# Performance work log

Measured on AMD Instinct MI355X. Metric: run time of the kernel, lower is better.

The kernel has to match this reference:

```python
import jax, jax.numpy as jnp
import numpy as np

N = 256    # b_s == nq == h*q == h*v (forced by the module's reshape/matmul constraints)
A = 1024   # model dim 'a'
K_DIM = 1  # self.k (h*k must equal 1 for the .view to be valid)


def setup_inputs() -> dict:
    key = jax.random.key(0)
    ks = jax.random.split(key, 5)
    s = 0.02
    x = jax.random.normal(ks[0], (N, N, A), dtype=jnp.float32)
    Wq = jax.random.normal(ks[1], (N, A), dtype=jnp.float32) * s      # fc_q: a -> h*q = N
    bq = jnp.zeros((N,), dtype=jnp.float32)
    Wk = jax.random.normal(ks[2], (K_DIM, A), dtype=jnp.float32) * s  # fc_k: a -> h*k = 1
    bk = jnp.zeros((K_DIM,), dtype=jnp.float32)
    Wv = jax.random.normal(ks[3], (N, A), dtype=jnp.float32) * s      # fc_v: a -> h*v = N
    bv = jnp.zeros((N,), dtype=jnp.float32)
    Wo = jax.random.normal(ks[4], (A, N), dtype=jnp.float32) * s      # fc_o: h*v -> a
    bo = jnp.zeros((A,), dtype=jnp.float32)
    return {"x": x, "Wq": Wq, "bq": bq, "Wk": Wk, "bk": bk,
            "Wv": Wv, "bv": bv, "Wo": Wo, "bo": bo}


def reference(x, Wq, bq, Wk, bk, Wv, bv, Wo, bo):
    # q = fc_q(x): (b_s, nq, h*q)
    q = jnp.einsum('bna,qa->bnq', x, Wq) + bq
    # k = fc_k(x).view(b_s, nq).permute(1, 0): (nq, b_s)
    klin = (jnp.einsum('bna,ka->bnk', x, Wk) + bk)[..., 0]  # (b_s, nq)
    kT = klin.T                                             # (nq, b_s)
    # att = matmul(kT, q) / sqrt(self.k): 2D kT broadcast over batch of q
    att = jnp.einsum('nm,bmq->bnq', kT, q) / np.sqrt(np.float32(K_DIM))
    att = jax.nn.softmax(att, axis=-1)  # dropout = identity (eval mode)
    # v = fc_v(x): (b_s, nq, h*v)
    v = jnp.einsum('bna,va->bnv', x, Wv) + bv
    # out = matmul(v, att): batched (nq, h*v) @ (nq, h*q) with h*v == nq
    out = jnp.einsum('bnm,bmq->bnq', v, att)
    # fc_o: (..., h*v) -> (..., a)
    return jnp.einsum('bnv,av->bna', out, Wo) + bo
```

## Files before the change

kernel.cpp:

```cpp
#include <hip/hip_runtime.h>


typedef unsigned short u16;
typedef unsigned int   uint;
using f32x4  = __attribute__((ext_vector_type(4))) float;
using bf16x8 = __attribute__((ext_vector_type(8))) short;
using u16x4  = __attribute__((ext_vector_type(4))) u16;

#define DEVI static __device__ __forceinline__

DEVI u16 f2bf(float f){
  union { float f; uint u; } v; v.f = f;
  uint r = v.u + 0x7fffu + ((v.u >> 16) & 1u);
  return (u16)(r >> 16);
}
DEVI float bf2f(u16 h){
  union { uint u; float f; } v; v.u = ((uint)h) << 16;
  return v.f;
}

typedef const uint __attribute__((address_space(1)))* as1_cuintp;
typedef uint __attribute__((address_space(3)))* as3_uintp;

DEVI void gl_lds16(const void* g, void* l){
  __builtin_amdgcn_global_load_lds((as1_cuintp)g, (as3_uintp)l, 16, 0, 0);
}

template<int ROWS, int NW>
DEVI void stage_tile(const u16* __restrict__ g, long long rowStride,
                     u16* lds, int lane, int wave){
  constexpr int NLD = ROWS >> 3;
  #pragma unroll
  for (int j = 0; j < NLD/NW; ++j){
    int r0  = (wave + NW*j) << 3;
    int row = r0 + (lane >> 3);
    const u16* src = g + (long long)row * rowStride
                       + (((lane & 7) ^ (lane >> 3)) << 3);
    gl_lds16(src, lds + r0 * 64);
  }
}

DEVI bf16x8 ldfrag(const u16* s, int rbase, int kk, int lane){
  int row = rbase + (lane & 15);
  int c   = (kk << 2) + (lane >> 4);
  return *(const bf16x8*)(s + row*64 + ((c ^ (row & 7)) << 3));
}

__global__ __launch_bounds__(512, 2)
void k_qvkl(const float* __restrict__ x,
            const u16* __restrict__ Wqh, const u16* __restrict__ Wql,
            const u16* __restrict__ Wvh,
            const float* __restrict__ Wk, const float* __restrict__ bk,
            const float* __restrict__ bq, const float* __restrict__ bv,
            u16* __restrict__ qTh, u16* __restrict__ qTl,
            u16* __restrict__ vout,
            u16* __restrict__ klTh, u16* __restrict__ klTl)
{
  __shared__ __align__(16) u16 sX [128*64];
  __shared__ __align__(16) u16 sXl[128*64];
  __shared__ __align__(16) u16 sQh[256*64];
  __shared__ __align__(16) u16 sQl[256*64];
  __shared__ __align__(16) u16 sV [256*64];

  const int tid  = threadIdx.x;
  const int lane = tid & 63;
  const int wave = tid >> 6;
  const int wm   = wave >> 2;
  const int wn   = wave & 3;
  const int tileM = blockIdx.x << 7;

  f32x4 qacc[4][4], vacc[4][4];
  #pragma unroll
  for (int i=0;i<4;i++)
    #pragma unroll
    for (int j=0;j<4;j++){
      qacc[i][j][0]=0.f; qacc[i][j][1]=0.f; qacc[i][j][2]=0.f; qacc[i][j][3]=0.f;
      vacc[i][j][0]=0.f; vacc[i][j][1]=0.f; vacc[i][j][2]=0.f; vacc[i][j][3]=0.f;
    }
  float kacc[4] = {0.f, 0.f, 0.f, 0.f};

  f32x4 xr[4];
  #pragma unroll
  for (int j=0;j<4;j++){
    int f = tid + (j << 9);
    xr[j] = *(const f32x4*)(x + (long long)(tileM + (f >> 4))*1024 + ((f & 15) << 2));
  }

  for (int kt = 0; kt < 1024; kt += 64){
    #pragma unroll
    for (int j=0;j<4;j++){
      int f   = tid + (j << 9);
      int row = f >> 4;
      int c16 = f & 15;
      f32x4 t = xr[j];
      u16x4 h4, l4;
      #pragma unroll
      for (int e=0;e<4;e++){
        u16 h = f2bf(t[e]);
        h4[e] = h;
        l4[e] = f2bf(t[e] - bf2f(h));
      }
      int off = row*64 + (((c16 >> 1) ^ (row & 7)) << 3) + ((c16 & 1) << 2);
      *(u16x4*)(sX  + off) = h4;
      *(u16x4*)(sXl + off) = l4;
      f32x4 w = *(const f32x4*)(Wk + kt + (c16 << 2));
      kacc[j] += t[0]*w[0] + t[1]*w[1] + t[2]*w[2] + t[3]*w[3];
    }
    stage_tile<256,8>(Wqh + kt, 1024, sQh, lane, wave);
    stage_tile<256,8>(Wql + kt, 1024, sQl, lane, wave);
    stage_tile<256,8>(Wvh + kt, 1024, sV , lane, wave);
    __syncthreads();

    if (kt < 960){
      #pragma unroll
      for (int j=0;j<4;j++){
        int f = tid + (j << 9);
        xr[j] = *(const f32x4*)(x + (long long)(tileM + (f >> 4))*1024
                                + (kt + 64) + ((f & 15) << 2));
      }
    }

    #pragma unroll
    for (int kk=0;kk<2;kk++){
      bf16x8 a[4], al[4];
      #pragma unroll
      for (int i=0;i<4;i++){
        a[i]  = ldfrag(sX , wm*64 + i*16, kk, lane);
        al[i] = ldfrag(sXl, wm*64 + i*16, kk, lane);
      }
      {
        bf16x8 b[4];
        #pragma unroll
        for (int i=0;i<4;i++) b[i] = ldfrag(sQh, wn*64 + i*16, kk, lane);
        #pragma unroll
        for (int mt=0;mt<4;mt++)
          #pragma unroll
          for (int nt=0;nt<4;nt++){
            qacc[mt][nt] = __builtin_amdgcn_mfma_f32_16x16x32_bf16(a[mt],  b[nt], qacc[mt][nt], 0,0,0);
            qacc[mt][nt] = __builtin_amdgcn_mfma_f32_16x16x32_bf16(al[mt], b[nt], qacc[mt][nt], 0,0,0);
          }
      }
      {
        bf16x8 b[4];
        #pragma unroll
        for (int i=0;i<4;i++) b[i] = ldfrag(sQl, wn*64 + i*16, kk, lane);
        #pragma unroll
        for (int mt=0;mt<4;mt++)
          #pragma unroll
          for (int nt=0;nt<4;nt++)
            qacc[mt][nt] = __builtin_amdgcn_mfma_f32_16x16x32_bf16(a[mt], b[nt], qacc[mt][nt], 0,0,0);
      }
      {
        bf16x8 b[4];
        #pragma unroll
        for (int i=0;i<4;i++) b[i] = ldfrag(sV, wn*64 + i*16, kk, lane);
        #pragma unroll
        for (int mt=0;mt<4;mt++)
          #pragma unroll
          for (int nt=0;nt<4;nt++)
            vacc[mt][nt] = __builtin_amdgcn_mfma_f32_16x16x32_bf16(a[mt], b[nt], vacc[mt][nt], 0,0,0);
      }
    }
    __syncthreads();
  }

  #pragma unroll
  for (int j=0;j<4;j++){
    #pragma unroll
    for (int m=1;m<16;m<<=1) kacc[j] += __shfl_xor(kacc[j], m, 64);
  }
  if ((lane & 15) == 0){
    #pragma unroll
    for (int j=0;j<4;j++){
      int f = tid + (j << 9);
      int r = tileM + (f >> 4);
      float kv = kacc[j] + bk[0];
      u16 h = f2bf(kv);
      klTh[(r & 255)*256 + (r >> 8)] = h;
      klTl[(r & 255)*256 + (r >> 8)] = f2bf(kv - bf2f(h));
    }
  }

  #pragma unroll
  for (int mt=0;mt<4;mt++)
    #pragma unroll
    for (int nt=0;nt<4;nt++){
      const int gr = tileM + wm*64 + mt*16 + ((lane >> 4) << 2);
      const int gc = wn*64 + nt*16 + (lane & 15);
      {
        const int bidx = gr >> 8, m = gr & 255;
        const long long off = ((long long)bidx << 16) + ((long long)gc << 8) + m;
        const float bb = bq[gc];
        u16x4 h4, l4;
        f32x4 v = qacc[mt][nt];
        #pragma unroll
        for (int r=0;r<4;r++){
          float fq = v[r] + bb;
          u16 h = f2bf(fq);
          h4[r] = h;
          l4[r] = f2bf(fq - bf2f(h));
        }
        *(u16x4*)(qTh + off) = h4;
        *(u16x4*)(qTl + off) = l4;
      }
      {
        const float bb = bv[gc];
        u16* o = vout + (long long)gr * 256 + gc;
        f32x4 v = vacc[mt][nt];
        #pragma unroll
        for (int r=0;r<4;r++) o[(long long)r * 256] = f2bf(v[r] + bb);
      }
    }
}

template<int WMODE>
__global__ __launch_bounds__(256, 2)
void k_gemm(const u16* __restrict__ Ag,
            const u16* __restrict__ Bhg,
            int N, int K, int tnCount, long long bStrideB,
            const float* __restrict__ bias,
            void* __restrict__ Co)
{
  __shared__ __align__(16) u16 sA[128*64];
  __shared__ __align__(16) u16 sB[128*64];

  const int tid  = threadIdx.x;
  const int lane = tid & 63;
  const int wave = tid >> 6;
  const int wm   = wave >> 1;
  const int wn   = wave & 1;
  const int tn   = blockIdx.x % tnCount;
  const int tm   = blockIdx.x / tnCount;
  const int tileM = tm << 7;
  const int tileN = tn << 7;

  const long long bOff = bStrideB ? (long long)(tileM >> 8) * bStrideB : 0;
  const u16* Bh_t = Bhg + bOff + (long long)tileN * K;

  f32x4 acc[4][4];
  #pragma unroll
  for (int i=0;i<4;i++)
    #pragma unroll
    for (int j=0;j<4;j++){
      acc[i][j][0]=0.f; acc[i][j][1]=0.f; acc[i][j][2]=0.f; acc[i][j][3]=0.f;
    }

  for (int kt = 0; kt < K; kt += 64){
    stage_tile<128,4>(Ag + (long long)tileM * K + kt, K, sA, lane, wave);
    stage_tile<128,4>(Bh_t + kt, K, sB, lane, wave);
    __syncthreads();
    #pragma unroll
    for (int kk=0;kk<2;kk++){
      bf16x8 a[4], b[4];
      #pragma unroll
      for (int i=0;i<4;i++){
        a[i] = ldfrag(sA, wm*64 + i*16, kk, lane);
        b[i] = ldfrag(sB, wn*64 + i*16, kk, lane);
      }
      #pragma unroll
      for (int mt=0;mt<4;mt++)
        #pragma unroll
        for (int nt=0;nt<4;nt++)
          acc[mt][nt] = __builtin_amdgcn_mfma_f32_16x16x32_bf16(a[mt], b[nt], acc[mt][nt], 0,0,0);
    }
    __syncthreads();
  }

  #pragma unroll
  for (int mt=0;mt<4;mt++)
    #pragma unroll
    for (int nt=0;nt<4;nt++){
      const int gr = tileM + wm*64 + mt*16 + ((lane >> 4) << 2);
      const int gc = tileN + wn*64 + nt*16 + (lane & 15);
      const float bb = bias ? bias[gc] : 0.f;
      f32x4 v = acc[mt][nt];
      if (WMODE == 0){
        float* o = (float*)Co + (long long)gr * N + gc;
        #pragma unroll
        for (int r=0;r<4;r++) o[(long long)r * N] = v[r] + bb;
      } else {
        u16* o = (u16*)Co + (long long)gr * N + gc;
        #pragma unroll
        for (int r=0;r<4;r++) o[(long long)r * N] = f2bf(v[r] + bb);
      }
    }
}

__global__ __launch_bounds__(256, 1)
void k_logits(const u16* __restrict__ qTh, const u16* __restrict__ qTl,
              const u16* __restrict__ klTh, const u16* __restrict__ klTl,
              u16* __restrict__ attT)
{
  __shared__ __align__(16) union U {
    struct S { u16 Ah[64*64]; u16 Al[64*64]; u16 Bh[256*64]; u16 Bl[256*64]; } s;
    float L[64*260];
  } u;
  __shared__ float rmax[64], rinv[64];

  const int tid  = threadIdx.x;
  const int lane = tid & 63;
  const int wave = tid >> 6;
  const int bidx  = blockIdx.x >> 2;
  const int ntile = blockIdx.x & 3;

  f32x4 acc[4][4];
  #pragma unroll
  for (int i=0;i<4;i++)
    #pragma unroll
    for (int j=0;j<4;j++){
      acc[i][j][0]=0.f; acc[i][j][1]=0.f; acc[i][j][2]=0.f; acc[i][j][3]=0.f;
    }

  for (int kt=0; kt<256; kt+=64){
    stage_tile<64,4> (klTh + (ntile << 6)*256 + kt, 256, u.s.Ah, lane, wave);
    stage_tile<64,4> (klTl + (ntile << 6)*256 + kt, 256, u.s.Al, lane, wave);
    stage_tile<256,4>(qTh + ((long long)bidx << 16) + kt, 256, u.s.Bh, lane, wave);
    stage_tile<256,4>(qTl + ((long long)bidx << 16) + kt, 256, u.s.Bl, lane, wave);
    __syncthreads();
    #pragma unroll
    for (int kk=0;kk<2;kk++){
      bf16x8 a[4], al[4], b[4], bl[4];
      #pragma unroll
      for (int i=0;i<4;i++){
        a[i]  = ldfrag(u.s.Ah, i*16, kk, lane);
        al[i] = ldfrag(u.s.Al, i*16, kk, lane);
        b[i]  = ldfrag(u.s.Bh, wave*64 + i*16, kk, lane);
        bl[i] = ldfrag(u.s.Bl, wave*64 + i*16, kk, lane);
      }
      #pragma unroll
      for (int mt=0;mt<4;mt++)
        #pragma unroll
        for (int nt=0;nt<4;nt++){
          acc[mt][nt] = __builtin_amdgcn_mfma_f32_16x16x32_bf16(a[mt],  b[nt],  acc[mt][nt], 0,0,0);
          acc[mt][nt] = __builtin_amdgcn_mfma_f32_16x16x32_bf16(al[mt], b[nt],  acc[mt][nt], 0,0,0);
          acc[mt][nt] = __builtin_amdgcn_mfma_f32_16x16x32_bf16(a[mt],  bl[nt], acc[mt][nt], 0,0,0);
        }
    }
    __syncthreads();
  }

  #pragma unroll
  for (int mt=0;mt<4;mt++)
    #pragma unroll
    for (int nt=0;nt<4;nt++){
      const int r0 = mt*16 + ((lane >> 4) << 2);
      const int c  = wave*64 + nt*16 + (lane & 15);
      #pragma unroll
      for (int r=0;r<4;r++) u.L[(r0 + r)*260 + c] = acc[mt][nt][r];
    }
  __syncthreads();

  {
    const int row = tid >> 2, sub = tid & 3;
    const float* Lr = &u.L[row*260 + sub*64];
    float mx = -3.4e38f;
    for (int i=0;i<64;i++) mx = fmaxf(mx, Lr[i]);
    mx = fmaxf(mx, __shfl_xor(mx, 1, 64));
    mx = fmaxf(mx, __shfl_xor(mx, 2, 64));
    float s = 0.f;
    for (int i=0;i<64;i++) s += __expf(Lr[i] - mx);
    s += __shfl_xor(s, 1, 64);
    s += __shfl_xor(s, 2, 64);
    if (sub == 0){ rmax[row] = mx; rinv[row] = 1.f / s; }
  }
  __syncthreads();

  {
    const int qq = tid;
    u16* dst = attT + ((long long)bidx << 16) + qq*256 + (ntile << 6);
    #pragma unroll
    for (int n0=0;n0<64;n0+=8){
      bf16x8 pk;
      #pragma unroll
      for (int e=0;e<8;e++){
        int n = n0 + e;
        float v = __expf(u.L[n*260 + qq] - rmax[n]) * rinv[n];
        pk[e] = (short)f2bf(v);
      }
      *(bf16x8*)(dst + n0) = pk;
    }
  }
}

__global__ void k_split(const float* __restrict__ w, u16* __restrict__ hi,
                        u16* __restrict__ lo, int n4){
  int i = blockIdx.x * blockDim.x + threadIdx.x;
  if (i >= n4) return;
  f32x4 v = ((const f32x4*)w)[i];
  u16x4 h, l;
  #pragma unroll
  for (int e=0;e<4;e++){
    u16 hh = f2bf(v[e]);
    h[e] = hh;
    l[e] = f2bf(v[e] - bf2f(hh));
  }
  ((u16x4*)hi)[i] = h;
  ((u16x4*)lo)[i] = l;
}

extern "C" void kernel_launch(void* const* d_in, const int* in_sizes, int n_in,
                              void* d_out, int out_size, void* d_ws, size_t ws_size,
                              hipStream_t stream){
  (void)in_sizes; (void)n_in; (void)out_size; (void)ws_size;
  const float* x  = (const float*)d_in[0];
  const float* Wq = (const float*)d_in[1];
  const float* bq = (const float*)d_in[2];
  const float* Wk = (const float*)d_in[3];
  const float* bk = (const float*)d_in[4];
  const float* Wv = (const float*)d_in[5];
  const float* bv = (const float*)d_in[6];
  const float* Wo = (const float*)d_in[7];
  const float* bo = (const float*)d_in[8];

  char* ob = (char*)d_out;
  u16* qTh  = (u16*)(ob);
  u16* qTl  = (u16*)(ob + (size_t)33554432);
  u16* vh   = (u16*)(ob + (size_t)67108864);
  u16* attT = (u16*)(ob + (size_t)100663296);
  char* wb = (char*)d_ws;
  u16* omh  = (u16*)(wb);
  u16* Wqh  = (u16*)(wb + (size_t)33554432);
  u16* Wql  = Wqh + 262144;
  u16* Wvh  = Wql + 262144;
  u16* Wvl  = Wvh + 262144;
  u16* Woh  = Wvl + 262144;
  u16* Wol  = Woh + 262144;
  u16* klTh = Wol + 262144;
  u16* klTl = klTh + 65536;

  k_split<<<256, 256, 0, stream>>>(Wq, Wqh, Wql, 65536);
  k_split<<<256, 256, 0, stream>>>(Wv, Wvh, Wvl, 65536);
  k_split<<<256, 256, 0, stream>>>(Wo, Woh, Wol, 65536);

  k_qvkl<<<512, 512, 0, stream>>>(x, Wqh, Wql, Wvh, Wk, bk, bq, bv,
                                  qTh, qTl, vh, klTh, klTl);
  k_logits<<<1024, 256, 0, stream>>>(qTh, qTl, klTh, klTl, attT);
  k_gemm<1><<<1024, 256, 0, stream>>>(vh, attT, 256, 256, 2, 65536, nullptr, omh);
  k_gemm<0><<<4096, 256, 0, stream>>>(omh, Woh, 1024, 256, 8, 0, bo, d_out);
}
```

Before: 354.4 us.

## Double-buffer weight tiles in halves to overlap async staging with MFMA

The QV projection kernel now splits each 256-column weight tile into two 128-column halves held in a double-buffered LDS array. The next half is staged asynchronously while the current half feeds the MFMAs, using manual vmcnt waits and raw barriers. X is loaded per iteration instead of prefetched into registers a step ahead. The intent is to hide global-to-LDS latency of the weights behind compute. It adds an extra barrier pair per K-step and relies on hand-tuned waitcnt values matching the number of outstanding loads.

```diff
diff --git a/kernel.cpp b/kernel.cpp
--- a/kernel.cpp
+++ b/kernel.cpp
@@ -58,9 +58,7 @@
 {
   __shared__ __align__(16) u16 sX [128*64];
   __shared__ __align__(16) u16 sXl[128*64];
-  __shared__ __align__(16) u16 sQh[256*64];
-  __shared__ __align__(16) u16 sQl[256*64];
-  __shared__ __align__(16) u16 sV [256*64];
+  __shared__ __align__(16) u16 sW [2][3*128*64];
 
   const int tid  = threadIdx.x;
   const int lane = tid & 63;
@@ -79,89 +77,106 @@
     }
   float kacc[4] = {0.f, 0.f, 0.f, 0.f};
 
-  f32x4 xr[4];
-  #pragma unroll
-  for (int j=0;j<4;j++){
-    int f = tid + (j << 9);
-    xr[j] = *(const f32x4*)(x + (long long)(tileM + (f >> 4))*1024 + ((f & 15) << 2));
-  }
+  stage_tile<128,8>(Wqh + 0, 1024, sW[0],         lane, wave);
+  stage_tile<128,8>(Wql + 0, 1024, sW[0] + 8192,  lane, wave);
+  stage_tile<128,8>(Wvh + 0, 1024, sW[0] + 16384, lane, wave);
 
   for (int kt = 0; kt < 1024; kt += 64){
     #pragma unroll
-    for (int j=0;j<4;j++){
-      int f   = tid + (j << 9);
-      int row = f >> 4;
-      int c16 = f & 15;
-      f32x4 t = xr[j];
-      u16x4 h4, l4;
-      #pragma unroll
-      for (int e=0;e<4;e++){
-        u16 h = f2bf(t[e]);
-        h4[e] = h;
-        l4[e] = f2bf(t[e] - bf2f(h));
-      }
-      int off = row*64 + (((c16 >> 1) ^ (row & 7)) << 3) + ((c16 & 1) << 2);
-      *(u16x4*)(sX  + off) = h4;
-      *(u16x4*)(sXl + off) = l4;
-      f32x4 w = *(const f32x4*)(Wk + kt + (c16 << 2));
-      kacc[j] += t[0]*w[0] + t[1]*w[1] + t[2]*w[2] + t[3]*w[3];
-    }
-    stage_tile<256,8>(Wqh + kt, 1024, sQh, lane, wave);
-    stage_tile<256,8>(Wql + kt, 1024, sQl, lane, wave);
-    stage_tile<256,8>(Wvh + kt, 1024, sV , lane, wave);
-    __syncthreads();
-
-    if (kt < 960){
-      #pragma unroll
-      for (int j=0;j<4;j++){
-        int f = tid + (j << 9);
-        xr[j] = *(const f32x4*)(x + (long long)(tileM + (f >> 4))*1024
-                                + (kt + 64) + ((f & 15) << 2));
-      }
-    }
-
-    #pragma unroll
-    for (int kk=0;kk<2;kk++){
-      bf16x8 a[4], al[4];
-      #pragma unroll
-      for (int i=0;i<4;i++){
-        a[i]  = ldfrag(sX , wm*64 + i*16, kk, lane);
-        al[i] = ldfrag(sXl, wm*64 + i*16, kk, lane);
-      }
+    for (int h = 0; h < 2; ++h){
+      f32x4 xr[4];
+      if (h == 0){
+        #pragma unroll
+        for (int j=0;j<4;j++){
+          int f = tid + (j << 9);
+          xr[j] = *(const f32x4*)(x + (long long)(tileM + (f >> 4))*1024
+                                  + kt + ((f & 15) << 2));
+        }
+        __builtin_amdgcn_sched_barrier(0);
+      }
+      const bool last = (kt == 960) && (h == 1);
+      if (!last){
+        const int nh  = h ^ 1;
+        const int nkt = (h == 0) ? kt : kt + 64;
+        u16* wb = sW[h ^ 1];
+        stage_tile<128,8>(Wqh + (nh << 7)*1024 + nkt, 1024, wb,         lane, wave);
+        stage_tile<128,8>(Wql + (nh << 7)*1024 + nkt, 1024, wb + 8192,  lane, wave);
+        stage_tile<128,8>(Wvh + (nh << 7)*1024 + nkt, 1024, wb + 16384, lane, wave);
+      }
+      if (h == 0){
+        #pragma unroll
+        for (int j=0;j<4;j++){
+          int f   = tid + (j << 9);
+          int row = f >> 4;
+          int c16 = f & 15;
+          f32x4 t = xr[j];
+          u16x4 h4, l4;
+          #pragma unroll
+          for (int e=0;e<4;e++){
+            u16 hh = f2bf(t[e]);
+            h4[e] = hh;
+            l4[e] = f2bf(t[e] - bf2f(hh));
+          }
+          int off = row*64 + (((c16 >> 1) ^ (row & 7)) << 3) + ((c16 & 1) << 2);
+          *(u16x4*)(sX  + off) = h4;
+          *(u16x4*)(sXl + off) = l4;
+          f32x4 w = *(const f32x4*)(Wk + kt + (c16 << 2));
+          kacc[j] += t[0]*w[0] + t[1]*w[1] + t[2]*w[2] + t[3]*w[3];
+        }
+      }
+      if (!last) asm volatile("s_waitcnt vmcnt(6) lgkmcnt(0)" ::: "memory");
+      else       asm volatile("s_waitcnt vmcnt(0) lgkmcnt(0)" ::: "memory");
+      __builtin_amdgcn_s_barrier();
+      __builtin_amdgcn_sched_barrier(0);
+
       {
-        bf16x8 b[4];
-        #pragma unroll
-        for (int i=0;i<4;i++) b[i] = ldfrag(sQh, wn*64 + i*16, kk, lane);
-        #pragma unroll
-        for (int mt=0;mt<4;mt++)
+        const u16* wb = sW[h];
+        #pragma unroll
+        for (int kk=0;kk<2;kk++){
+          bf16x8 a[4], al[4];
           #pragma unroll
-          for (int nt=0;nt<4;nt++){
-            qacc[mt][nt] = __builtin_amdgcn_mfma_f32_16x16x32_bf16(a[mt],  b[nt], qacc[mt][nt], 0,0,0);
-            qacc[mt][nt] = __builtin_amdgcn_mfma_f32_16x16x32_bf16(al[mt], b[nt], qacc[mt][nt], 0,0,0);
+          for (int i=0;i<4;i++){
+            a[i]  = ldfrag(sX , wm*64 + i*16, kk, lane);
+            al[i] = ldfrag(sXl, wm*64 + i*16, kk, lane);
           }
-      }
-      {
-        bf16x8 b[4];
-        #pragma unroll
-        for (int i=0;i<4;i++) b[i] = ldfrag(sQl, wn*64 + i*16, kk, lane);
-        #pragma unroll
-        for (int mt=0;mt<4;mt++)
-          #pragma unroll
-          for (int nt=0;nt<4;nt++)
-            qacc[mt][nt] = __builtin_amdgcn_mfma_f32_16x16x32_bf16(a[mt], b[nt], qacc[mt][nt], 0,0,0);
-      }
-      {
-        bf16x8 b[4];
-        #pragma unroll
-        for (int i=0;i<4;i++) b[i] = ldfrag(sV, wn*64 + i*16, kk, lane);
-        #pragma unroll
-        for (int mt=0;mt<4;mt++)
-          #pragma unroll
-          for (int nt=0;nt<4;nt++)
-            vacc[mt][nt] = __builtin_amdgcn_mfma_f32_16x16x32_bf16(a[mt], b[nt], vacc[mt][nt], 0,0,0);
-      }
-    }
-    __syncthreads();
+          {
+            bf16x8 b[2];
+            #pragma unroll
+            for (int i=0;i<2;i++) b[i] = ldfrag(wb, wn*32 + i*16, kk, lane);
+            #pragma unroll
+            for (int mt=0;mt<4;mt++)
+              #pragma unroll
+              for (int ntl=0;ntl<2;ntl++){
+                qacc[mt][(h<<1)|ntl] = __builtin_amdgcn_mfma_f32_16x16x32_bf16(a[mt],  b[ntl], qacc[mt][(h<<1)|ntl], 0,0,0);
+                qacc[mt][(h<<1)|ntl] = __builtin_amdgcn_mfma_f32_16x16x32_bf16(al[mt], b[ntl], qacc[mt][(h<<1)|ntl], 0,0,0);
+              }
+          }
+          {
+            bf16x8 b[2];
+            #pragma unroll
+            for (int i=0;i<2;i++) b[i] = ldfrag(wb + 8192, wn*32 + i*16, kk, lane);
+            #pragma unroll
+            for (int mt=0;mt<4;mt++)
+              #pragma unroll
+              for (int ntl=0;ntl<2;ntl++)
+                qacc[mt][(h<<1)|ntl] = __builtin_amdgcn_mfma_f32_16x16x32_bf16(a[mt], b[ntl], qacc[mt][(h<<1)|ntl], 0,0,0);
+          }
+          {
+            bf16x8 b[2];
+            #pragma unroll
+            for (int i=0;i<2;i++) b[i] = ldfrag(wb + 16384, wn*32 + i*16, kk, lane);
+            #pragma unroll
+            for (int mt=0;mt<4;mt++)
+              #pragma unroll
+              for (int ntl=0;ntl<2;ntl++)
+                vacc[mt][(h<<1)|ntl] = __builtin_amdgcn_mfma_f32_16x16x32_bf16(a[mt], b[ntl], vacc[mt][(h<<1)|ntl], 0,0,0);
+          }
+        }
+      }
+      asm volatile("s_waitcnt lgkmcnt(0)" ::: "memory");
+      __builtin_amdgcn_s_barrier();
+      __builtin_amdgcn_sched_barrier(0);
+    }
   }
 
   #pragma unroll
@@ -175,30 +190,30 @@
       int f = tid + (j << 9);
       int r = tileM + (f >> 4);
       float kv = kacc[j] + bk[0];
-      u16 h = f2bf(kv);
-      klTh[(r & 255)*256 + (r >> 8)] = h;
-      klTl[(r & 255)*256 + (r >> 8)] = f2bf(kv - bf2f(h));
+      u16 hh = f2bf(kv);
+      klTh[(r & 255)*256 + (r >> 8)] = hh;
+      klTl[(r & 255)*256 + (r >> 8)] = f2bf(kv - bf2f(hh));
     }
   }
 
   #pragma unroll
   for (int mt=0;mt<4;mt++)
     #pragma unroll
-    for (int nt=0;nt<4;nt++){
+    for (int ntg=0;ntg<4;ntg++){
       const int gr = tileM + wm*64 + mt*16 + ((lane >> 4) << 2);
-      const int gc = wn*64 + nt*16 + (lane & 15);
+      const int gc = ((ntg >> 1) << 7) + wn*32 + ((ntg & 1) << 4) + (lane & 15);
       {
         const int bidx = gr >> 8, m = gr & 255;
         const long long off = ((long long)bidx << 16) + ((long long)gc << 8) + m;
         const float bb = bq[gc];
         u16x4 h4, l4;
-        f32x4 v = qacc[mt][nt];
+        f32x4 v = qacc[mt][ntg];
         #pragma unroll
         for (int r=0;r<4;r++){
           float fq = v[r] + bb;
-          u16 h = f2bf(fq);
-          h4[r] = h;
-          l4[r] = f2bf(fq - bf2f(h));
+          u16 hh = f2bf(fq);
+          h4[r] = hh;
+          l4[r] = f2bf(fq - bf2f(hh));
         }
         *(u16x4*)(qTh + off) = h4;
         *(u16x4*)(qTl + off) = l4;
@@ -206,7 +221,7 @@
       {
         const float bb = bv[gc];
         u16* o = vout + (long long)gr * 256 + gc;
-        f32x4 v = vacc[mt][nt];
+        f32x4 v = vacc[mt][ntg];
         #pragma unroll
         for (int r=0;r<4;r++) o[(long long)r * 256] = f2bf(v[r] + bb);
       }
```

Result: slower. 370.0 us (+4.4%).
